# Kernel tuning notes

Measured on AMD Instinct MI355X. Metric: run time of the kernel, lower is better.

Reference implementation:

```python
import jax, jax.numpy as jnp
import numpy as np

B = 16
H_DIM = 512
N_HEADS = 8
HEAD_DIM = H_DIM // N_HEADS  # 64
EPS = 1e-5
DST_LENS = 256 + 16 * np.arange(B)  # ragged dst sizes, total 6016
SRC_LENS = 512 - 8 * np.arange(B)   # ragged src sizes, total 7232


def _pad_info(lens):
    # gather/scatter indices to move between flat ragged layout and [B, Lmax, D]
    lens = np.asarray(lens)
    off = np.concatenate([[0], np.cumsum(lens)[:-1]])
    gid = np.repeat(np.arange(len(lens)), lens)
    pos = np.arange(int(lens.sum())) - np.repeat(off, lens)
    Lmax = int(lens.max())
    mask = jnp.asarray(np.arange(Lmax)[None, :] < lens[:, None])
    return gid, pos, Lmax, mask


def _bn(x, g, b):
    # BatchNorm1d forward with batch statistics (training-mode normalization)
    m = x.mean(0)
    v = ((x - m) ** 2).mean(0)
    return (x - m) / jnp.sqrt(v + EPS) * g + b


def setup_inputs() -> dict:
    key = jax.random.key(0)
    ks = jax.random.split(key, 20)
    total_src = int(SRC_LENS.sum())
    total_dst = int(DST_LENS.sum())
    w = lambda k, shape: jax.random.normal(k, shape, jnp.float32) * 0.02
    return {
        "src_h": jax.random.normal(ks[0], (total_src, H_DIM), jnp.float32),
        "dst_h": jax.random.normal(ks[1], (total_dst, H_DIM), jnp.float32),
        "src_num_verts": jnp.asarray(SRC_LENS, jnp.int32),
        "dst_num_verts": jnp.asarray(DST_LENS, jnp.int32),
        "Wq": w(ks[2], (H_DIM, H_DIM)), "bq": w(ks[3], (H_DIM,)),
        "Wk": w(ks[4], (H_DIM, H_DIM)), "bk": w(ks[5], (H_DIM,)),
        "Wv": w(ks[6], (H_DIM, H_DIM)), "bv": w(ks[7], (H_DIM,)),
        "Wm": w(ks[8], (H_DIM, H_DIM)), "bm": w(ks[9], (H_DIM,)),
        "W1": w(ks[10], (H_DIM, 2 * H_DIM)), "b1": w(ks[11], (H_DIM,)),
        "g1": jnp.ones((H_DIM,), jnp.float32), "be1": jnp.zeros((H_DIM,), jnp.float32),
        "W2": w(ks[12], (H_DIM, H_DIM)), "b2": w(ks[13], (H_DIM,)),
        "g2": jnp.ones((H_DIM,), jnp.float32), "be2": jnp.zeros((H_DIM,), jnp.float32),
    }


def reference(src_h, dst_h, src_num_verts, dst_num_verts,
              Wq, bq, Wk, bk, Wv, bv, Wm, bm,
              W1, b1, g1, be1, W2, b2, g2, be2):
    s_lens = np.asarray(src_num_verts)
    d_lens = np.asarray(dst_num_verts)
    sg, sp, Ls, smask = _pad_info(s_lens)
    dg, dp, Ld, dmask = _pad_info(d_lens)

    # ragged -> padded [B, L, D]
    src_pad = jnp.zeros((B, Ls, H_DIM), src_h.dtype).at[sg, sp].set(src_h)
    dst_pad = jnp.zeros((B, Ld, H_DIM), dst_h.dtype).at[dg, dp].set(dst_h)

    # Conv1d(k=1) projections; channel c = d*num_heads + h -> reshape (head_dim, n_heads)
    q = (dst_pad @ Wq.T + bq).reshape(B, Ld, HEAD_DIM, N_HEADS)
    k = (src_pad @ Wk.T + bk).reshape(B, Ls, HEAD_DIM, N_HEADS)
    v = (src_pad @ Wv.T + bv).reshape(B, Ls, HEAD_DIM, N_HEADS)

    scores = jnp.einsum('bndh,bmdh->bhnm', q, k) / 8.0  # sqrt(head_dim)=8
    scores = jnp.where(smask[:, None, None, :], scores, -1e9)
    attn = jax.nn.softmax(scores, axis=-1)
    o = jnp.einsum('bhnm,bmdh->bndh', attn, v).reshape(B, Ld, H_DIM)
    o = o @ Wm.T + bm  # merge Conv1d(k=1)

    # padded -> ragged
    h_msg = o[dg, dp]  # [total_dst, h_dim]

    h = dst_h
    x = jnp.concatenate([h, h_msg], axis=-1)
    x = _bn(x @ W1.T + b1, g1, be1)
    x = jax.nn.relu(x)
    x = _bn(x @ W2.T + b2, g2, be2)
    return h + x
```

## Files before the change

kernel.cpp:

```cpp
#include <hip/hip_runtime.h>
#include <hip/hip_bf16.h>

#define H_DIM 512
#define N_HEADS 8
#define HEAD_DIM 64
#define NBATCH 16

typedef __attribute__((ext_vector_type(8))) short short8;
typedef __attribute__((ext_vector_type(4))) float floatx4;

typedef unsigned short us16;

#define SW3(r) ((((r) >> 1) & 3) | (((r) & 1) << 2))

__device__ inline unsigned short f2bf(float f) {
  unsigned int u = __float_as_uint(f);
  unsigned int r = (u + 0x7fffu + ((u >> 16) & 1u)) >> 16;
  return (unsigned short)r;
}

__device__ inline void gld16(const us16* g, us16* l) {
  __builtin_amdgcn_global_load_lds(
      (const __attribute__((address_space(1))) void*)g,
      (__attribute__((address_space(3))) void*)l, 16, 0, 0);
}

__global__ __launch_bounds__(256) void prep_all(
    const float* __restrict__ src_h, const float* __restrict__ dst_h,
    const float* __restrict__ Wq, const float* __restrict__ Wk,
    const float* __restrict__ Wv, const float* __restrict__ W1,
    const float* __restrict__ W2, const float* __restrict__ Wm,
    const float* __restrict__ b1, const float* __restrict__ bm,
    us16* __restrict__ src_bf, us16* __restrict__ dst_bf,
    us16* __restrict__ Wqb, us16* __restrict__ Wkv, us16* __restrict__ Wf,
    us16* __restrict__ W2b, float* __restrict__ b1p, float* __restrict__ st,
    int n_src, int n_dst) {
  __shared__ __align__(16) us16 As[64 * 48];
  __shared__ __align__(16) us16 Bs[64 * 48];
  const int blk = blockIdx.x;
  const int t = threadIdx.x;

  if (blk < 2048) {
    if (blk == 0) {
      float4 z = make_float4(0.f, 0.f, 0.f, 0.f);
      ((float4*)st)[t] = z;
      ((float4*)st)[t + 256] = z;
    }
    const float* srcs[7] = {src_h, dst_h, Wq, Wk, Wv, W1, W2};
    us16* dsts[7] = {src_bf, dst_bf, Wqb, Wkv, Wkv + 262144, Wf, W2b};
    int ns[7] = {n_src, n_dst, 262144, 262144, 262144, 262144, 262144};
    for (int rg = 0; rg < 7; ++rg) {
      const float* sp = srcs[rg];
      us16* dp = dsts[rg];
      const bool strided = (rg == 5);
      for (int i = (blk * 256 + t) * 4; i < ns[rg]; i += 2048 * 256 * 4) {
        int j = strided ? ((i >> 9) * 1024 + (i & 511)) : i;
        float4 v = *(const float4*)(sp + j);
        ushort4 o;
        o.x = f2bf(v.x); o.y = f2bf(v.y); o.z = f2bf(v.z); o.w = f2bf(v.w);
        *(ushort4*)(dp + j) = o;
      }
    }
  } else if (blk < 2112) {
    const int bx = (blk - 2048) & 7, byk = (blk - 2048) >> 3;
    const int w = t >> 6, lane = t & 63;
    const int lane15 = lane & 15, quad = lane >> 4;
    const int wm = w >> 1, wn = w & 1;
    const int bn_ = bx * 64, bk = byk * 64;
    floatx4 acc[2][2];
#pragma unroll
    for (int a = 0; a < 2; ++a)
#pragma unroll
      for (int c = 0; c < 2; ++c) acc[a][c] = (floatx4){0.f, 0.f, 0.f, 0.f};
    for (int j0 = 0; j0 < 512; j0 += 32) {
      {
        int n = t >> 2, jj0 = (t & 3) * 8;
        const float* rp = W1 + (size_t)(bn_ + n) * 1024 + 512 + j0 + jj0;
        float4 va = *(const float4*)(rp);
        float4 vb = *(const float4*)(rp + 4);
        ushort4 pa, pb;
        pa.x = f2bf(va.x); pa.y = f2bf(va.y); pa.z = f2bf(va.z); pa.w = f2bf(va.w);
        pb.x = f2bf(vb.x); pb.y = f2bf(vb.y); pb.z = f2bf(vb.z); pb.w = f2bf(vb.w);
        *(ushort4*)(As + n * 48 + jj0) = pa;
        *(ushort4*)(As + n * 48 + jj0 + 4) = pb;
      }
      {
        int jj = t >> 3, kc0 = (t & 7) * 8;
        const float* rp = Wm + (size_t)(j0 + jj) * 512 + bk + kc0;
        float4 va = *(const float4*)(rp);
        float4 vb = *(const float4*)(rp + 4);
        float vv[8] = {va.x, va.y, va.z, va.w, vb.x, vb.y, vb.z, vb.w};
#pragma unroll
        for (int e = 0; e < 8; ++e) Bs[(kc0 + e) * 48 + jj] = f2bf(vv[e]);
      }
      __syncthreads();
      short8 a_[2], b_[2];
#pragma unroll
      for (int mt = 0; mt < 2; ++mt)
        a_[mt] = *(const short8*)(As + (wm * 32 + mt * 16 + lane15) * 48 + quad * 8);
#pragma unroll
      for (int nt = 0; nt < 2; ++nt)
        b_[nt] = *(const short8*)(Bs + (wn * 32 + nt * 16 + lane15) * 48 + quad * 8);
#pragma unroll
      for (int mt = 0; mt < 2; ++mt)
#pragma unroll
        for (int nt = 0; nt < 2; ++nt)
          acc[mt][nt] = __builtin_amdgcn_mfma_f32_16x16x32_bf16(
              a_[mt], b_[nt], acc[mt][nt], 0, 0, 0);
      __syncthreads();
    }
#pragma unroll
    for (int mt = 0; mt < 2; ++mt) {
      int n0 = bn_ + wm * 32 + mt * 16 + quad * 4;
#pragma unroll
      for (int nt = 0; nt < 2; ++nt) {
        int k = bk + wn * 32 + nt * 16 + lane15;
#pragma unroll
        for (int r = 0; r < 4; ++r)
          Wf[(size_t)(n0 + r) * 1024 + 512 + k] = f2bf(acc[mt][nt][r]);
      }
    }
  } else {
    int n = (blk - 2112) * 256 + t;
    if (n < 512) {
      const float* rp = W1 + (size_t)n * 1024 + 512;
      float s = 0.f;
      for (int j = 0; j < 512; j += 4) {
        float4 a = *(const float4*)(rp + j);
        float4 c = *(const float4*)(bm + j);
        s += a.x * c.x + a.y * c.y + a.z * c.z + a.w * c.w;
      }
      b1p[n] = b1[n] + s;
    }
  }
}

__device__ inline void gemm_body(
    const us16* __restrict__ A1, const us16* __restrict__ A2,
    const us16* __restrict__ W,
    const float* __restrict__ bias0, const float* __restrict__ bias1,
    void* __restrict__ C0, void* __restrict__ C1, float* __restrict__ stats,
    int M, int N, int K, int mode, int bx, int by) {
  __shared__ __align__(16) us16 As[3 * 64 * 64];
  __shared__ __align__(16) us16 Bs[3 * 128 * 64];
  const int t = threadIdx.x, w = t >> 6, lane = t & 63;
  const int lane15 = lane & 15, quad = lane >> 4;
  const int bm = bx * 64, bn = by * 128;
  const int lrow = lane >> 3;
  const int sl = lane & 7;

  floatx4 acc[4][2];
#pragma unroll
  for (int a = 0; a < 4; ++a)
#pragma unroll
    for (int c = 0; c < 2; ++c) acc[a][c] = (floatx4){0.f, 0.f, 0.f, 0.f};

  const int nk = K >> 6;

#define ISSUE(i, b)                                                          \
  {                                                                          \
    int k0 = (i) << 6;                                                       \
    const us16* Ab = (k0 < 512) ? A1 : A2;                                   \
    int ka = k0 & 511;                                                       \
    _Pragma("unroll")                                                        \
    for (int p = 0; p < 2; ++p) {                                            \
      int rbase = p * 32 + w * 8;                                            \
      int row = rbase + lrow;                                                \
      int kg = sl ^ SW3(row);                                                \
      gld16(Ab + (size_t)(bm + row) * 512 + ka + kg * 8,                     \
            As + (b) * 4096 + rbase * 64);                                   \
    }                                                                        \
    _Pragma("unroll")                                                        \
    for (int p = 0; p < 4; ++p) {                                            \
      int rbase = p * 32 + w * 8;                                            \
      int row = rbase + lrow;                                                \
      int kg = sl ^ SW3(row);                                                \
      gld16(W + (size_t)(bn + row) * K + k0 + kg * 8,                        \
            Bs + (b) * 8192 + rbase * 64);                                   \
    }                                                                        \
  }

  ISSUE(0, 0);
  if (nk > 1) ISSUE(1, 1);
  int cur = 0;
  for (int i = 0; i < nk; ++i) {
    if (i + 1 < nk) {
      asm volatile("s_waitcnt vmcnt(6)" ::: "memory");
    } else {
      asm volatile("s_waitcnt vmcnt(0)" ::: "memory");
    }
    __builtin_amdgcn_s_barrier();
    asm volatile("" ::: "memory");
    if (i + 2 < nk) {
      int nb = cur + 2;
      if (nb >= 3) nb -= 3;
      ISSUE(i + 2, nb);
    }
#pragma unroll
    for (int kh = 0; kh < 2; ++kh) {
      const int g = kh * 4 + quad;
      short8 a_[4], b_[2];
#pragma unroll
      for (int mt = 0; mt < 4; ++mt) {
        int r = mt * 16 + lane15;
        a_[mt] = *(const short8*)(As + cur * 4096 + r * 64 + (g ^ SW3(r)) * 8);
      }
#pragma unroll
      for (int nt = 0; nt < 2; ++nt) {
        int c = w * 32 + nt * 16 + lane15;
        b_[nt] = *(const short8*)(Bs + cur * 8192 + c * 64 + (g ^ SW3(c)) * 8);
      }
#pragma unroll
      for (int mt = 0; mt < 4; ++mt)
#pragma unroll
        for (int nt = 0; nt < 2; ++nt)
          acc[mt][nt] = __builtin_amdgcn_mfma_f32_16x16x32_bf16(
              a_[mt], b_[nt], acc[mt][nt], 0, 0, 0);
    }
    cur = (cur == 2) ? 0 : cur + 1;
  }
#undef ISSUE

  if (mode == 0) {
#pragma unroll
    for (int nt = 0; nt < 2; ++nt) {
      int col = bn + w * 32 + nt * 16 + lane15;
      float bv = bias0[col];
      float s = 0.f, qq = 0.f;
#pragma unroll
      for (int mt = 0; mt < 4; ++mt) {
        int row0 = bm + mt * 16 + quad * 4;
#pragma unroll
        for (int r = 0; r < 4; ++r) {
          float val = acc[mt][nt][r] + bv;
          ((float*)C0)[(size_t)(row0 + r) * N + col] = val;
          s += val; qq = fmaf(val, val, qq);
        }
      }
      s += __shfl_xor(s, 16); s += __shfl_xor(s, 32);
      qq += __shfl_xor(qq, 16); qq += __shfl_xor(qq, 32);
      if (quad == 0) {
        atomicAdd(&stats[col], s);
        atomicAdd(&stats[512 + col], qq);
      }
    }
  } else if (mode == 1) {
#pragma unroll
    for (int nt = 0; nt < 2; ++nt) {
      int col = bn + w * 32 + nt * 16 + lane15;
      float bv = bias0[col];
      int hh = col & 7, dd = col >> 3;
#pragma unroll
      for (int mt = 0; mt < 4; ++mt) {
        int row0 = bm + mt * 16 + quad * 4;
#pragma unroll
        for (int r = 0; r < 4; ++r)
          ((us16*)C0)[((size_t)hh * M + row0 + r) * 64 + dd] = f2bf(acc[mt][nt][r] + bv);
      }
    }
  } else {
#pragma unroll
    for (int nt = 0; nt < 2; ++nt) {
      int col = bn + w * 32 + nt * 16 + lane15;
      if (col < 512) {
        float bv = bias0[col];
        int hh = col & 7, dd = col >> 3;
#pragma unroll
        for (int mt = 0; mt < 4; ++mt) {
          int row0 = bm + mt * 16 + quad * 4;
#pragma unroll
          for (int r = 0; r < 4; ++r)
            ((us16*)C0)[((size_t)hh * M + row0 + r) * 64 + dd] = f2bf(acc[mt][nt][r] + bv);
        }
      } else {
        int cv = col - 512;
        float bv = bias1[cv];
        int plane = (cv & 7) * 64 + (cv >> 3);
#pragma unroll
        for (int mt = 0; mt < 4; ++mt) {
          int row0 = bm + mt * 16 + quad * 4;
          ushort4 pk;
          pk.x = f2bf(acc[mt][nt][0] + bv);
          pk.y = f2bf(acc[mt][nt][1] + bv);
          pk.z = f2bf(acc[mt][nt][2] + bv);
          pk.w = f2bf(acc[mt][nt][3] + bv);
          *(ushort4*)((us16*)C1 + (size_t)plane * M + row0) = pk;
        }
      }
    }
  }
}

__global__ __launch_bounds__(256) void gemm_ffn(
    const us16* __restrict__ A1, const us16* __restrict__ A2,
    const us16* __restrict__ W,
    const float* __restrict__ bias0, void* __restrict__ C0,
    float* __restrict__ stats, int M, int K) {
  int b = blockIdx.x;
  int i = (b & 7) * ((int)gridDim.x >> 3) + (b >> 3);
  gemm_body(A1, A2, W, bias0, nullptr, C0, nullptr, stats, M, 512, K, 0,
            i >> 2, i & 3);
}

__global__ __launch_bounds__(256) void gemm_qkv(
    const us16* __restrict__ dst_bf, const us16* __restrict__ src_bf,
    const us16* __restrict__ Wqb, const us16* __restrict__ Wkv,
    const float* __restrict__ bq, const float* __restrict__ bk,
    const float* __restrict__ bv,
    us16* __restrict__ Qh, us16* __restrict__ Kh, us16* __restrict__ Vt,
    int Md, int Ms) {
  int b = blockIdx.x;
  int i = (b & 7) * ((int)gridDim.x >> 3) + (b >> 3);
  int nq = (Md / 64) * 4;
  if (i < nq) {
    gemm_body(dst_bf, dst_bf, Wqb, bq, nullptr, Qh, nullptr, nullptr,
              Md, 512, 512, 1, i >> 2, i & 3);
  } else {
    int j = i - nq;
    gemm_body(src_bf, src_bf, Wkv, bk, bv, Kh, Vt, nullptr,
              Ms, 1024, 512, 4, j >> 3, j & 7);
  }
}

__global__ __launch_bounds__(256) void attn_v6(
    const us16* __restrict__ Qh, const us16* __restrict__ Kh,
    const us16* __restrict__ Vt, const int* __restrict__ dlens,
    const int* __restrict__ slens, us16* __restrict__ O,
    int Md, int Ms) {
  const int b = blockIdx.x, h = blockIdx.y, tile = blockIdx.z;
  int doff = 0, soff = 0;
  for (int i = 0; i < NBATCH; ++i)
    if (i < b) { doff += dlens[i]; soff += slens[i]; }
  const int dlen = dlens[b], slen = slens[b];
  if (tile * 64 >= dlen) return;

  __shared__ __align__(16) us16 Ks[2 * 64 * 64];
  __shared__ __align__(16) us16 Vts[2 * 64 * 64];
  __shared__ __align__(16) us16 Pw[4][16 * 72];

  const int t = threadIdx.x, wv = t >> 6, lane = t & 63;
  const int lane15 = lane & 15, quad = lane >> 4;
  const int i0w = tile * 64 + wv * 16;
  const bool active = i0w < dlen;

  const us16* Qp = Qh + ((size_t)h * Md + doff + (active ? i0w : 0)) * 64;
  const us16* Kp = Kh + ((size_t)h * Ms + soff) * 64;
  const us16* Vtp = Vt + ((size_t)h * 64) * Ms + soff;

  short8 af0 = *(const short8*)(Qp + (size_t)lane15 * 64 + quad * 8);
  short8 af1 = *(const short8*)(Qp + (size_t)lane15 * 64 + 32 + quad * 8);

  floatx4 oa[4];
#pragma unroll
  for (int nt = 0; nt < 4; ++nt) oa[nt] = (floatx4){0.f, 0.f, 0.f, 0.f};
  float m_r[4] = {-3.0e38f, -3.0e38f, -3.0e38f, -3.0e38f};
  float l_r[4] = {0.f, 0.f, 0.f, 0.f};

  const int nc = (slen + 63) >> 6;

#define KVST(c, bu)                                                       \
  {                                                                       \
    int jb = (c) << 6;                                                    \
    _Pragma("unroll")                                                     \
    for (int p = 0; p < 2; ++p) {                                         \
      int row = wv * 16 + p * 8 + (lane >> 3);                            \
      int slt = lane & 7;                                                 \
      int kg = slt ^ SW3(row);                                            \
      gld16(Kp + (size_t)(jb + row) * 64 + kg * 8,                        \
            Ks + (bu) * 4096 + (wv * 16 + p * 8) * 64);                   \
      gld16(Vtp + (size_t)row * Ms + jb + kg * 8,                         \
            Vts + (bu) * 4096 + (wv * 16 + p * 8) * 64);                  \
    }                                                                     \
  }

  KVST(0, 0);
  if (nc > 1) KVST(1, 1);
  for (int c = 0; c < nc; ++c) {
    const int cur = c & 1;
    if (c + 1 < nc) {
      asm volatile("s_waitcnt vmcnt(4)" ::: "memory");
    } else {
      asm volatile("s_waitcnt vmcnt(0)" ::: "memory");
    }
    __builtin_amdgcn_s_barrier();
    asm volatile("" ::: "memory");

    if (active) {
      const int j0 = c << 6;
      floatx4 s[4];
#pragma unroll
      for (int jt = 0; jt < 4; ++jt) {
        int j = jt * 16 + lane15;
        short8 b0 = *(const short8*)(Ks + cur * 4096 + j * 64 + ((quad ^ SW3(j)) * 8));
        short8 b1 = *(const short8*)(Ks + cur * 4096 + j * 64 + (((4 + quad) ^ SW3(j)) * 8));
        floatx4 a = (floatx4){0.f, 0.f, 0.f, 0.f};
        a = __builtin_amdgcn_mfma_f32_16x16x32_bf16(af0, b0, a, 0, 0, 0);
        a = __builtin_amdgcn_mfma_f32_16x16x32_bf16(af1, b1, a, 0, 0, 0);
        s[jt] = a;
      }
      float mx[4] = {-3.0e38f, -3.0e38f, -3.0e38f, -3.0e38f};
#pragma unroll
      for (int jt = 0; jt < 4; ++jt) {
        bool valid = (j0 + jt * 16 + lane15) < slen;
#pragma unroll
        for (int r = 0; r < 4; ++r) {
          float v = valid ? s[jt][r] * 0.125f : -3.0e38f;
          s[jt][r] = v;
          mx[r] = fmaxf(mx[r], v);
        }
      }
#pragma unroll
      for (int r = 0; r < 4; ++r) {
        mx[r] = fmaxf(mx[r], __shfl_xor(mx[r], 1));
        mx[r] = fmaxf(mx[r], __shfl_xor(mx[r], 2));
        mx[r] = fmaxf(mx[r], __shfl_xor(mx[r], 4));
        mx[r] = fmaxf(mx[r], __shfl_xor(mx[r], 8));
      }
      float al[4], sum[4];
#pragma unroll
      for (int r = 0; r < 4; ++r) {
        float mn = fmaxf(m_r[r], mx[r]);
        al[r] = __expf(m_r[r] - mn);
        m_r[r] = mn;
        sum[r] = 0.f;
      }
#pragma unroll
      for (int jt = 0; jt < 4; ++jt)
#pragma unroll
        for (int r = 0; r < 4; ++r) {
          float e = __expf(s[jt][r] - m_r[r]);
          sum[r] += e;
          Pw[wv][(quad * 4 + r) * 72 + jt * 16 + lane15] = f2bf(e);
        }
#pragma unroll
      for (int r = 0; r < 4; ++r) {
        sum[r] += __shfl_xor(sum[r], 1);
        sum[r] += __shfl_xor(sum[r], 2);
        sum[r] += __shfl_xor(sum[r], 4);
        sum[r] += __shfl_xor(sum[r], 8);
        l_r[r] = l_r[r] * al[r] + sum[r];
      }
#pragma unroll
      for (int nt = 0; nt < 4; ++nt)
#pragma unroll
        for (int r = 0; r < 4; ++r) oa[nt][r] *= al[r];
      short8 pa0 = *(const short8*)(&Pw[wv][lane15 * 72 + quad * 8]);
      short8 pa1 = *(const short8*)(&Pw[wv][lane15 * 72 + 32 + quad * 8]);
#pragma unroll
      for (int nt = 0; nt < 4; ++nt) {
        int d = nt * 16 + lane15;
        short8 v0 = *(const short8*)(Vts + cur * 4096 + d * 64 + ((quad ^ SW3(d)) * 8));
        short8 v1 = *(const short8*)(Vts + cur * 4096 + d * 64 + (((4 + quad) ^ SW3(d)) * 8));
        oa[nt] = __builtin_amdgcn_mfma_f32_16x16x32_bf16(pa0, v0, oa[nt], 0, 0, 0);
        oa[nt] = __builtin_amdgcn_mfma_f32_16x16x32_bf16(pa1, v1, oa[nt], 0, 0, 0);
      }
    }

    asm volatile("" ::: "memory");
    __builtin_amdgcn_s_barrier();
    asm volatile("" ::: "memory");
    if (c + 2 < nc) KVST(c + 2, cur);
  }
#undef KVST

  if (active) {
    float linv[4];
#pragma unroll
    for (int r = 0; r < 4; ++r) linv[r] = 1.f / l_r[r];
#pragma unroll
    for (int r = 0; r < 4; ++r) {
      int i = quad * 4 + r;
      us16* orow = O + (size_t)(doff + i0w + i) * H_DIM + h;
#pragma unroll
      for (int nt = 0; nt < 4; ++nt) {
        int d = nt * 16 + lane15;
        orow[d * 8] = f2bf(oa[nt][r] * linv[r]);
      }
    }
  }
}

__global__ __launch_bounds__(256) void bn_apply(
    const float* __restrict__ X, const float* __restrict__ stats,
    const float* __restrict__ g, const float* __restrict__ be,
    const float* __restrict__ resid, void* __restrict__ Y,
    int M, float invM, int relu, int out_bf) {
  const size_t total = (size_t)M * H_DIM;
  for (size_t i = (size_t)blockIdx.x * 256 + threadIdx.x; i < total;
       i += (size_t)gridDim.x * 256) {
    int c = (int)(i & (H_DIM - 1));
    float mean = stats[c] * invM;
    float var = fmaf(-mean, mean, stats[H_DIM + c] * invM);
    float x = X[i];
    float y = (x - mean) * rsqrtf(var + 1e-5f) * g[c] + be[c];
    if (relu) y = fmaxf(y, 0.f);
    if (resid) y += resid[i];
    if (out_bf) ((us16*)Y)[i] = f2bf(y);
    else ((float*)Y)[i] = y;
  }
}

extern "C" void kernel_launch(void* const* d_in, const int* in_sizes, int n_in,
                              void* d_out, int out_size, void* d_ws, size_t ws_size,
                              hipStream_t stream) {
  const float* src_h = (const float*)d_in[0];
  const float* dst_h = (const float*)d_in[1];
  const int* s_lens  = (const int*)d_in[2];
  const int* d_lens  = (const int*)d_in[3];
  const float* Wq = (const float*)d_in[4];  const float* bq = (const float*)d_in[5];
  const float* Wk = (const float*)d_in[6];  const float* bk = (const float*)d_in[7];
  const float* Wv = (const float*)d_in[8];  const float* bv = (const float*)d_in[9];
  const float* Wm = (const float*)d_in[10]; const float* bm = (const float*)d_in[11];
  const float* W1 = (const float*)d_in[12]; const float* b1 = (const float*)d_in[13];
  const float* g1 = (const float*)d_in[14]; const float* be1 = (const float*)d_in[15];
  const float* W2 = (const float*)d_in[16]; const float* b2 = (const float*)d_in[17];
  const float* g2 = (const float*)d_in[18]; const float* be2 = (const float*)d_in[19];

  const int total_src = in_sizes[0] / H_DIM;
  const int total_dst = in_sizes[1] / H_DIM;

  char* ws = (char*)d_ws;
  us16* src_bf = (us16*)(ws + 0);
  us16* dst_bf = (us16*)(ws + 7405568);
  us16* wbf    = (us16*)(ws + 13565952);
  float* b1p   = (float*)(ws + 16711680);
  us16* Qh     = (us16*)(ws + 17235968);
  us16* Kh     = (us16*)(ws + 23396352);
  us16* Vt     = (us16*)(ws + 30801920);
  us16* Ob     = (us16*)(ws + 38207488);
  us16* X1bf   = (us16*)(ws + 44367872);
  float* st    = (float*)(ws + 50528256);
  float* X1    = (float*)(ws + 17235968);
  float* X2    = (float*)(ws + 30801920);
  float* st1 = st, *st2 = st + 1024;

  us16* Wqb = wbf;
  us16* Wkv = wbf + 262144;
  us16* Wf  = wbf + 786432;
  us16* W2b = wbf + 1310720;

  const int mbd = total_dst / 64;
  const int mbs = total_src / 64;
  const dim3 blk256(256);

  prep_all<<<dim3(2114), blk256, 0, stream>>>(
      src_h, dst_h, Wq, Wk, Wv, W1, W2, Wm, b1, bm,
      src_bf, dst_bf, Wqb, Wkv, Wf, W2b, b1p, st,
      total_src * H_DIM, total_dst * H_DIM);

  gemm_qkv<<<dim3(mbd * 4 + mbs * 8), blk256, 0, stream>>>(
      dst_bf, src_bf, Wqb, Wkv, bq, bk, bv, Qh, Kh, Vt, total_dst, total_src);

  attn_v6<<<dim3(NBATCH, N_HEADS, 8), blk256, 0, stream>>>(
      Qh, Kh, Vt, d_lens, s_lens, Ob, total_dst, total_src);

  gemm_ffn<<<dim3(mbd * 4), blk256, 0, stream>>>(
      dst_bf, Ob, Wf, b1p, X1, st1, total_dst, 1024);

  bn_apply<<<dim3(512), blk256, 0, stream>>>(X1, st1, g1, be1, nullptr, X1bf,
                                             total_dst, 1.f / (float)total_dst, 1, 1);

  gemm_ffn<<<dim3(mbd * 4), blk256, 0, stream>>>(
      X1bf, X1bf, W2b, b2, X2, st2, total_dst, 512);

  bn_apply<<<dim3(512), blk256, 0, stream>>>(X2, st2, g2, be2, dst_h, d_out,
                                             total_dst, 1.f / (float)total_dst, 0, 0);
}
```

Before: 258.3 us.

## Permute Q/K weight rows to head-major and shrink GEMM pipeline to double buffer

Wq and Wk rows, and the matching Wm-folded columns of W1, are permuted during the bf16 conversion so Q and K outputs come out head-contiguous in a plain row-major [M,512] layout. This replaces the scattered per-head strided stores in the GEMM epilogue with contiguous stores. The attention kernel now reads Q/K with a 512 stride, and its output is written head-contiguous. Separately, the GEMM's LDS ring drops from triple to double buffering with an extra barrier before the next prefetch, cutting LDS use at the cost of less load/compute overlap.

```diff
diff --git a/kernel.cpp b/kernel.cpp
--- a/kernel.cpp
+++ b/kernel.cpp
@@ -12,6 +12,9 @@
 typedef unsigned short us16;
 
 #define SW3(r) ((((r) >> 1) & 3) | (((r) & 1) << 2))
+
+#define PERMC(c) ((((c) & 7) << 6) | ((c) >> 3))
+#define IPERMC(cp) ((((cp) & 63) << 3) | ((cp) >> 6))
 
 __device__ inline unsigned short f2bf(float f) {
   unsigned int u = __float_as_uint(f);
@@ -49,16 +52,27 @@
     const float* srcs[7] = {src_h, dst_h, Wq, Wk, Wv, W1, W2};
     us16* dsts[7] = {src_bf, dst_bf, Wqb, Wkv, Wkv + 262144, Wf, W2b};
     int ns[7] = {n_src, n_dst, 262144, 262144, 262144, 262144, 262144};
+    const int md_[7] = {0, 0, 2, 2, 0, 1, 0};
     for (int rg = 0; rg < 7; ++rg) {
       const float* sp = srcs[rg];
       us16* dp = dsts[rg];
-      const bool strided = (rg == 5);
+      const int mode = md_[rg];
       for (int i = (blk * 256 + t) * 4; i < ns[rg]; i += 2048 * 256 * 4) {
-        int j = strided ? ((i >> 9) * 1024 + (i & 511)) : i;
-        float4 v = *(const float4*)(sp + j);
+        int js, jd;
+        if (mode == 1) {
+          js = ((i >> 9) * 1024) + (i & 511);
+          jd = js;
+        } else if (mode == 2) {
+          int r = i >> 9;
+          js = i;
+          jd = (PERMC(r) << 9) + (i & 511);
+        } else {
+          js = i; jd = i;
+        }
+        float4 v = *(const float4*)(sp + js);
         ushort4 o;
         o.x = f2bf(v.x); o.y = f2bf(v.y); o.z = f2bf(v.z); o.w = f2bf(v.w);
-        *(ushort4*)(dp + j) = o;
+        *(ushort4*)(dp + jd) = o;
       }
     }
   } else if (blk < 2112) {
@@ -115,9 +129,10 @@
 #pragma unroll
       for (int nt = 0; nt < 2; ++nt) {
         int k = bk + wn * 32 + nt * 16 + lane15;
+        int kp = PERMC(k);
 #pragma unroll
         for (int r = 0; r < 4; ++r)
-          Wf[(size_t)(n0 + r) * 1024 + 512 + k] = f2bf(acc[mt][nt][r]);
+          Wf[(size_t)(n0 + r) * 1024 + 512 + kp] = f2bf(acc[mt][nt][r]);
       }
     }
   } else {
@@ -141,8 +156,8 @@
     const float* __restrict__ bias0, const float* __restrict__ bias1,
     void* __restrict__ C0, void* __restrict__ C1, float* __restrict__ stats,
     int M, int N, int K, int mode, int bx, int by) {
-  __shared__ __align__(16) us16 As[3 * 64 * 64];
-  __shared__ __align__(16) us16 Bs[3 * 128 * 64];
+  __shared__ __align__(16) us16 As[2 * 64 * 64];
+  __shared__ __align__(16) us16 Bs[2 * 128 * 64];
   const int t = threadIdx.x, w = t >> 6, lane = t & 63;
   const int lane15 = lane & 15, quad = lane >> 4;
   const int bm = bx * 64, bn = by * 128;
@@ -182,8 +197,8 @@
 
   ISSUE(0, 0);
   if (nk > 1) ISSUE(1, 1);
-  int cur = 0;
   for (int i = 0; i < nk; ++i) {
+    const int cur = i & 1;
     if (i + 1 < nk) {
       asm volatile("s_waitcnt vmcnt(6)" ::: "memory");
     } else {
@@ -191,11 +206,6 @@
     }
     __builtin_amdgcn_s_barrier();
     asm volatile("" ::: "memory");
-    if (i + 2 < nk) {
-      int nb = cur + 2;
-      if (nb >= 3) nb -= 3;
-      ISSUE(i + 2, nb);
-    }
 #pragma unroll
     for (int kh = 0; kh < 2; ++kh) {
       const int g = kh * 4 + quad;
@@ -217,7 +227,10 @@
           acc[mt][nt] = __builtin_amdgcn_mfma_f32_16x16x32_bf16(
               a_[mt], b_[nt], acc[mt][nt], 0, 0, 0);
     }
-    cur = (cur == 2) ? 0 : cur + 1;
+    asm volatile("" ::: "memory");
+    __builtin_amdgcn_s_barrier();
+    asm volatile("" ::: "memory");
+    if (i + 2 < nk) ISSUE(i + 2, cur);
   }
 #undef ISSUE
 
@@ -248,14 +261,13 @@
 #pragma unroll
     for (int nt = 0; nt < 2; ++nt) {
       int col = bn + w * 32 + nt * 16 + lane15;
-      float bv = bias0[col];
-      int hh = col & 7, dd = col >> 3;
+      float bv = bias0[IPERMC(col)];
 #pragma unroll
       for (int mt = 0; mt < 4; ++mt) {
         int row0 = bm + mt * 16 + quad * 4;
 #pragma unroll
         for (int r = 0; r < 4; ++r)
-          ((us16*)C0)[((size_t)hh * M + row0 + r) * 64 + dd] = f2bf(acc[mt][nt][r] + bv);
+          ((us16*)C0)[(size_t)(row0 + r) * 512 + col] = f2bf(acc[mt][nt][r] + bv);
       }
     }
   } else {
@@ -263,14 +275,13 @@
     for (int nt = 0; nt < 2; ++nt) {
       int col = bn + w * 32 + nt * 16 + lane15;
       if (col < 512) {
-        float bv = bias0[col];
-        int hh = col & 7, dd = col >> 3;
+        float bv = bias0[IPERMC(col)];
 #pragma unroll
         for (int mt = 0; mt < 4; ++mt) {
           int row0 = bm + mt * 16 + quad * 4;
 #pragma unroll
           for (int r = 0; r < 4; ++r)
-            ((us16*)C0)[((size_t)hh * M + row0 + r) * 64 + dd] = f2bf(acc[mt][nt][r] + bv);
+            ((us16*)C0)[(size_t)(row0 + r) * 512 + col] = f2bf(acc[mt][nt][r] + bv);
         }
       } else {
         int cv = col - 512;
@@ -343,12 +354,12 @@
   const int i0w = tile * 64 + wv * 16;
   const bool active = i0w < dlen;
 
-  const us16* Qp = Qh + ((size_t)h * Md + doff + (active ? i0w : 0)) * 64;
-  const us16* Kp = Kh + ((size_t)h * Ms + soff) * 64;
+  const us16* Qp = Qh + ((size_t)(doff + (active ? i0w : 0))) * 512 + h * 64;
+  const us16* Kp = Kh + ((size_t)soff) * 512 + h * 64;
   const us16* Vtp = Vt + ((size_t)h * 64) * Ms + soff;
 
-  short8 af0 = *(const short8*)(Qp + (size_t)lane15 * 64 + quad * 8);
-  short8 af1 = *(const short8*)(Qp + (size_t)lane15 * 64 + 32 + quad * 8);
+  short8 af0 = *(const short8*)(Qp + (size_t)lane15 * 512 + quad * 8);
+  short8 af1 = *(const short8*)(Qp + (size_t)lane15 * 512 + 32 + quad * 8);
 
   floatx4 oa[4];
 #pragma unroll
@@ -366,7 +377,7 @@
       int row = wv * 16 + p * 8 + (lane >> 3);                            \
       int slt = lane & 7;                                                 \
       int kg = slt ^ SW3(row);                                            \
-      gld16(Kp + (size_t)(jb + row) * 64 + kg * 8,                        \
+      gld16(Kp + (size_t)(jb + row) * 512 + kg * 8,                       \
             Ks + (bu) * 4096 + (wv * 16 + p * 8) * 64);                   \
       gld16(Vtp + (size_t)row * Ms + jb + kg * 8,                         \
             Vts + (bu) * 4096 + (wv * 16 + p * 8) * 64);                  \
@@ -470,11 +481,11 @@
 #pragma unroll
     for (int r = 0; r < 4; ++r) {
       int i = quad * 4 + r;
-      us16* orow = O + (size_t)(doff + i0w + i) * H_DIM + h;
+      us16* orow = O + (size_t)(doff + i0w + i) * H_DIM + h * 64;
 #pragma unroll
       for (int nt = 0; nt < 4; ++nt) {
         int d = nt * 16 + lane15;
-        orow[d * 8] = f2bf(oa[nt][r] * linv[r]);
+        orow[d] = f2bf(oa[nt][r] * linv[r]);
       }
     }
   }
```

Result: faster. 237.1 us (-8.2%).
